# Optimization experiments

Hardware: AMD Instinct MI355X
Metric: run time of the kernel (lower is better)

Reference implementation:

```python
import jax, jax.numpy as jnp
import numpy as np

WINDOW = 1
BETA = 0.01
EPS = 1e-6


def conv3x3(x, W, b):
    y = jax.lax.conv_general_dilated(x, W, (1, 1), 'SAME',
                                     dimension_numbers=('NCHW', 'OIHW', 'NCHW'))
    return y + b[None, :, None, None]


def grid_sample_bilinear(feat, gx, gy):
    # feat [n,C,H,W]; gx,gy [n,h,w] normalized to [-1,1]; align_corners=True, zeros padding
    n, C, H, W = feat.shape
    ix = (gx + 1.0) * 0.5 * (W - 1)
    iy = (gy + 1.0) * 0.5 * (H - 1)
    x0 = jnp.floor(ix)
    y0 = jnp.floor(iy)
    wx = ix - x0
    wy = iy - y0

    def corner(xc, yc, wgt):
        valid = (xc >= 0) & (xc <= W - 1) & (yc >= 0) & (yc <= H - 1)
        xi = jnp.clip(xc, 0, W - 1).astype(jnp.int32)
        yi = jnp.clip(yc, 0, H - 1).astype(jnp.int32)
        g = jax.vmap(lambda f, yy, xx: f[:, yy, xx])(feat, yi, xi)  # [n,C,h,w]
        return g * (wgt * valid)[:, None, :, :]

    return (corner(x0, y0, (1 - wx) * (1 - wy)) +
            corner(x0 + 1, y0, wx * (1 - wy)) +
            corner(x0, y0 + 1, (1 - wx) * wy) +
            corner(x0 + 1, y0 + 1, wx * wy))


def random_pooling(gt, rand, h, w):
    # adaptive_max_pool2d with exact-division output -> uniform block max pool
    n, c, H, W = gt.shape
    kh, kw = H // h, W // w
    rm = rand * (gt > 0.1)
    blocks = rm.reshape(n, c, h, kh, w, kw).transpose(0, 1, 2, 4, 3, 5)
    blocks = blocks.reshape(n, c, h, w, kh * kw)
    loc = jnp.argmax(blocks, axis=-1)
    bi, bj = loc // kw, loc % kw
    row = jnp.arange(h, dtype=jnp.int32)[:, None] * kh + bi
    col = jnp.arange(w, dtype=jnp.int32)[None, :] * kw + bj
    indices = row * W + col  # flat indices into H*W, [n,c,h,w]
    gtf = gt.reshape(n, c, H * W)
    rg = jnp.take_along_axis(gtf, indices.reshape(n, c, h * w), axis=-1)
    rg = rg.reshape(n, c, h, w)
    rg = jnp.where(rg < 0.1, 0.0, rg)
    return rg, indices


def log_grads(rg, window):
    # windowed log-gradients in 4 directions per offset distance
    n, c, h, w = rg.shape
    image = jnp.pad(rg, ((0, 0), (0, 0), (window, window), (window, window)))
    limg = jnp.log(image + EPS)
    mask = image > 0.1
    lc = limg[:, :, window:window + h, window:window + w]
    mc = mask[:, :, window:window + h, window:window + w]
    gs, ms = [], []
    for dd in range(1, window + 1):
        for ox, oy in ((0, dd), (dd, dd), (dd, 0), (dd, -dd)):
            sx, sy = window + ox, window + oy
            gs.append(lc - limg[:, :, sx:sx + h, sy:sy + w])
            ms.append(mc & mask[:, :, sx:sx + h, sy:sy + w])
    return jnp.concatenate(gs, 1), jnp.concatenate(ms, 1)


def single_loss(rand_i, x, d, gts, W_att, b_att, W_post, b_post):
    n, c, h, w = d.shape
    H, W = gts.shape[2], gts.shape[3]
    rg, indices = random_pooling(gts, rand_i, h, w)
    bias = W // w // 2 + (H // h // 2) * W
    indices = indices + bias
    ind_x = 2.0 * ((indices % W).astype(d.dtype) / W - 0.5)
    ind_y = 2.0 * ((indices // W).astype(d.dtype) / H - 0.5)
    feat = grid_sample_bilinear(x, ind_x[:, 0], ind_y[:, 0])
    att = jax.nn.sigmoid(conv3x3(feat, W_att, b_att))
    ds = conv3x3(att * d, W_post, b_post)
    grad_gt, grad_mk = log_grads(rg, WINDOW)
    a = jnp.abs(ds - grad_gt)
    sl1 = jnp.where(a < BETA, 0.5 * a * a / BETA, a - 0.5 * BETA)
    mk = grad_mk.astype(ds.dtype)
    return (sl1 * mk).sum() / mk.sum()


def setup_inputs() -> dict:
    key = jax.random.key(0)
    ks = jax.random.split(key, 8)
    n, H, W = 4, 480, 640
    h, w = 120, 160
    DC, FC, R = 32, 32, 20  # r = 5 * 4 * window
    return {
        'x': jax.random.normal(ks[0], (n, FC, H, W), dtype=jnp.float32),
        'd': jax.random.normal(ks[1], (n, DC, h, w), dtype=jnp.float32),
        'gts': jax.random.uniform(ks[2], (n, 1, H, W), dtype=jnp.float32),
        'rand': jax.random.uniform(ks[3], (R, n, 1, H, W), dtype=jnp.float32),
        'W_att': jax.random.normal(ks[4], (DC, FC, 3, 3), dtype=jnp.float32) * 0.05,
        'b_att': jnp.zeros((DC,), dtype=jnp.float32),
        'W_post': jax.random.normal(ks[5], (4 * WINDOW, DC, 3, 3), dtype=jnp.float32) * 0.05,
        'b_post': jnp.zeros((4 * WINDOW,), dtype=jnp.float32),
    }


def reference(x, d, gts, rand, W_att, b_att, W_post, b_post):
    def step(acc, r_i):
        return acc + single_loss(r_i, x, d, gts, W_att, b_att, W_post, b_post), None
    total, _ = jax.lax.scan(step, jnp.float32(0.0), rand)
    return total / rand.shape[0]
```

## Files before the change

### kernel.cpp

```cpp
#include <hip/hip_runtime.h>
#include <math.h>

#define NN 4
#define FC 32
#define DC 32
#define HH 480
#define WW 640
#define hh 120
#define ww 160
#define RR 20
#define TILE 14
#define ATT 16
#define FT 18
#define BIAS_IDX 1282
#define CP 16
#define PSTR 20
#define ASTR 257
#define LOGEPS -13.815511f
#define MTHR   -8.0f

#define WS_W1T 64
#define WS_W2T 9280
#define WS_WB1 10432
#define WS_WB2 15040
#define WS_RG  20480
#define WS_IDX 1556480
#define WS_XB  3092480
#define XB_COUNT ((size_t)NN * HH * WW * 16)
#define WS_NEED_BYTES (((size_t)WS_XB + XB_COUNT) * 4)

typedef __attribute__((ext_vector_type(8))) short short8;
typedef __attribute__((ext_vector_type(4))) float f32x4;

__device__ __forceinline__ unsigned int bf16pack(float a, float b) {
    unsigned int ua = __float_as_uint(a);
    ua = (ua + 0x7fffu + ((ua >> 16) & 1u)) >> 16;
    unsigned int ub = __float_as_uint(b);
    ub = (ub + 0x7fffu + ((ub >> 16) & 1u)) >> 16;
    return ua | (ub << 16);
}
__device__ __forceinline__ unsigned short bf16r(float f) {
    unsigned int u = __float_as_uint(f);
    u = (u + 0x7fffu + ((u >> 16) & 1u)) >> 16;
    return (unsigned short)u;
}
__device__ __forceinline__ float bf16tof(unsigned short s) {
    return __uint_as_float(((unsigned int)s) << 16);
}

__global__ void prep_kernel(const float* __restrict__ W_att, const float* __restrict__ W_post,
                            float* __restrict__ ws) {
    int tid = threadIdx.x;
    if (tid < 2*RR) ws[tid] = 0.f;
    float* w1t = ws + WS_W1T;
    float* w2t = ws + WS_W2T;
    for (int i = tid; i < 32*32*9; i += blockDim.x) {
        int oc = i / (32*9); int rem = i % (32*9); int c = rem / 9; int tap = rem % 9;
        w1t[(tap*32 + c)*32 + oc] = W_att[i];
    }
    for (int i = tid; i < 4*32*9; i += blockDim.x) {
        int oc = i / (32*9); int rem = i % (32*9); int c = rem / 9; int tap = rem % 9;
        w2t[(tap*32 + c)*4 + oc] = W_post[i];
    }
    unsigned int* wb = (unsigned int*)(ws + WS_WB1);
    for (int i = tid; i < 9*2*64; i += blockDim.x) {
        int lane = i & 63; int th = i >> 6;
        int t = th >> 1, h2 = th & 1;
        int q = lane >> 4, col = lane & 15, oc = h2*16 + col;
        unsigned int vv[4];
        #pragma unroll
        for (int j = 0; j < 4; ++j) {
            int c0 = 8*q + 2*j;
            float f0 = W_att[(oc*32 + c0    )*9 + t];
            float f1 = W_att[(oc*32 + c0 + 1)*9 + t];
            vv[j] = bf16pack(f0, f1);
        }
        uint4 v4; v4.x = vv[0]; v4.y = vv[1]; v4.z = vv[2]; v4.w = vv[3];
        ((uint4*)wb)[i] = v4;
    }
    unsigned int* wb2 = (unsigned int*)(ws + WS_WB2);
    for (int i = tid; i < 9*2*64; i += blockDim.x) {
        int lane = i & 63; int th = i >> 6;
        int t = th >> 1, part = th & 1;
        int q = lane >> 4, oc = lane & 15;
        unsigned int vv[4];
        #pragma unroll
        for (int j = 0; j < 4; ++j) {
            int c0 = 8*q + 2*j;
            float f0 = (oc < 4) ? W_post[(oc*32 + c0    )*9 + t] : 0.f;
            float f1 = (oc < 4) ? W_post[(oc*32 + c0 + 1)*9 + t] : 0.f;
            if (part == 0) {
                vv[j] = ((unsigned int)bf16r(f0)) | (((unsigned int)bf16r(f1)) << 16);
            } else {
                float l0 = f0 - bf16tof(bf16r(f0));
                float l1 = f1 - bf16tof(bf16r(f1));
                vv[j] = ((unsigned int)bf16r(l0)) | (((unsigned int)bf16r(l1)) << 16);
            }
        }
        uint4 v4; v4.x = vv[0]; v4.y = vv[1]; v4.z = vv[2]; v4.w = vv[3];
        ((uint4*)wb2)[i] = v4;
    }
}

__global__ void xpack_kernel(const float* __restrict__ x, unsigned int* __restrict__ xb) {
    const int y = blockIdx.x;
    const int n = blockIdx.y;
    for (int px = threadIdx.x; px < WW; px += 256) {
        unsigned int* o = xb + ((size_t)(n*HH + y)*WW + px) * 16;
        uint4 v[4];
        #pragma unroll
        for (int k = 0; k < 4; ++k) {
            #pragma unroll
            for (int j = 0; j < 4; ++j) {
                int cp = 4*k + j;
                float f0 = x[((size_t)(n*FC + 2*cp    )*HH + y)*WW + px];
                float f1 = x[((size_t)(n*FC + 2*cp + 1)*HH + y)*WW + px];
                ((unsigned int*)&v[k])[j] = bf16pack(f0, f1);
            }
        }
        #pragma unroll
        for (int k = 0; k < 4; ++k) ((uint4*)o)[k] = v[k];
    }
}

__global__ void pool_kernel(const float* __restrict__ gts, const float* __restrict__ rnd,
                            float* __restrict__ ws) {
    const int r = blockIdx.z, n = blockIdx.y;
    const int cell = blockIdx.x * 256 + threadIdx.x;
    const int h = cell / ww, w = cell % ww;
    const float* gt_n = gts + (size_t)n * HH * WW;
    const float* rd_n = rnd + ((size_t)r * NN + n) * (size_t)(HH * WW);
    float best = -1.f, bg = 0.f; int bii = 0, bjj = 0;
    #pragma unroll
    for (int bi = 0; bi < 4; ++bi) {
        const float4 g4 = *(const float4*)(gt_n + (size_t)(h*4 + bi)*WW + w*4);
        const float4 r4 = *(const float4*)(rd_n + (size_t)(h*4 + bi)*WW + w*4);
        const float gv[4] = {g4.x, g4.y, g4.z, g4.w};
        const float rv[4] = {r4.x, r4.y, r4.z, r4.w};
        #pragma unroll
        for (int bj = 0; bj < 4; ++bj) {
            float rm = (gv[bj] > 0.1f) ? rv[bj] : 0.f;
            if (rm > best) { best = rm; bii = bi; bjj = bj; bg = gv[bj]; }
        }
    }
    int idx_b = (h*4 + bii) * WW + (w*4 + bjj) + BIAS_IDX;
    size_t o = ((size_t)(r*NN + n) * (hh*ww)) + cell;
    float g2 = (bg < 0.1f) ? 0.f : bg;
    ((float*)(ws + WS_RG))[o] = logf(g2 + 1e-6f);
    ((unsigned int*)(ws + WS_IDX))[o] = ((unsigned int)(idx_b / WW) << 16) | (unsigned int)(idx_b % WW);
}

__launch_bounds__(256, 5)
__global__ void wvl_main(const unsigned int* __restrict__ xb, const float* __restrict__ d,
                         const float* __restrict__ b_att, const float* __restrict__ b_post,
                         float* __restrict__ ws) {
    __shared__ unsigned int s_feat[FT * FT * PSTR];
    __shared__ float s_plog[FT * FT];
    __shared__ int   s_pidx[FT * FT];
    __shared__ float s_rn[4], s_rd[4];

    const float* lg_all  = (const float*)(ws + WS_RG);
    const unsigned int* pidx_all = (const unsigned int*)(ws + WS_IDX);

    const int tid = threadIdx.x;

    const int f   = blockIdx.x;
    const int xcd = f & 7;
    const int bb  = f >> 3;
    const int gi  = bb / 120;
    const int ii  = bb % 120;
    const int band = gi * 8 + xcd;
    const int n   = band / 18;
    const int rem = band % 18;
    const int ty  = rem >> 1;
    const int tx  = (rem & 1) * 6 + (ii % 6);
    const int r   = ii / 6;

    const int py0 = ty * TILE - 2;
    const int px0 = tx * TILE - 2;

    {
        const size_t base = (size_t)(r*NN + n) * (hh*ww);
        for (int p = tid; p < FT * FT; p += 256) {
            int pi = p / FT, pj = p % FT;
            int gi2 = py0 + pi, gj = px0 + pj;
            float lval = LOGEPS; int pk = -1;
            if (gi2 >= 0 && gi2 < hh && gj >= 0 && gj < ww) {
                size_t o = base + (size_t)gi2 * ww + gj;
                lval = lg_all[o];
                pk = (int)pidx_all[o];
            }
            s_plog[p] = lval;
            s_pidx[p] = pk;
        }
    }
    __syncthreads();

    for (int p = tid; p < FT * FT; p += 256) {
        int pk = s_pidx[p];
        unsigned int* dst = &s_feat[p * PSTR];
        if (pk < 0) {
            uint4 z; z.x = z.y = z.z = z.w = 0u;
            #pragma unroll
            for (int k = 0; k < 4; ++k) ((uint4*)dst)[k] = z;
            continue;
        }
        int rr2 = pk >> 16;
        int cc  = pk & 0xffff;
        float gxf = 2.0f * ((float)cc  / (float)WW - 0.5f);
        float gyf = 2.0f * ((float)rr2 / (float)HH - 0.5f);
        float ix = (gxf + 1.0f) * 0.5f * (float)(WW - 1);
        float iy = (gyf + 1.0f) * 0.5f * (float)(HH - 1);
        float x0f = floorf(ix), y0f = floorf(iy);
        float wx = ix - x0f, wy = iy - y0f;
        int x0 = (int)x0f, y0 = (int)y0f;
        float vx0 = (x0f >= 0.f        && x0f <= (float)(WW-1)) ? 1.f : 0.f;
        float vx1 = (x0f + 1.f >= 0.f  && x0f + 1.f <= (float)(WW-1)) ? 1.f : 0.f;
        float vy0 = (y0f >= 0.f        && y0f <= (float)(HH-1)) ? 1.f : 0.f;
        float vy1 = (y0f + 1.f >= 0.f  && y0f + 1.f <= (float)(HH-1)) ? 1.f : 0.f;
        int xi0 = min(max(x0, 0), WW-1),  xi1 = min(max(x0+1, 0), WW-1);
        int yi0 = min(max(y0, 0), HH-1),  yi1 = min(max(y0+1, 0), HH-1);
        float w00 = (1.f-wx)*(1.f-wy) * (vx0*vy0);
        float w10 = wx*(1.f-wy)       * (vx1*vy0);
        float w01 = (1.f-wx)*wy       * (vx0*vy1);
        float w11 = wx*wy             * (vx1*vy1);
        const uint4* q00 = (const uint4*)(xb + ((size_t)(n*HH + yi0)*WW + xi0) * 16);
        const uint4* q10 = (const uint4*)(xb + ((size_t)(n*HH + yi0)*WW + xi1) * 16);
        const uint4* q01 = (const uint4*)(xb + ((size_t)(n*HH + yi1)*WW + xi0) * 16);
        const uint4* q11 = (const uint4*)(xb + ((size_t)(n*HH + yi1)*WW + xi1) * 16);
        #pragma unroll
        for (int k = 0; k < 4; ++k) {
            uint4 A = q00[k], B = q10[k], C = q01[k], D = q11[k];
            uint4 o;
            #pragma unroll
            for (int j = 0; j < 4; ++j) {
                unsigned int ua = ((const unsigned int*)&A)[j];
                unsigned int ub = ((const unsigned int*)&B)[j];
                unsigned int uc = ((const unsigned int*)&C)[j];
                unsigned int ud = ((const unsigned int*)&D)[j];
                float f0 = w00 * __uint_as_float(ua << 16)
                         + w10 * __uint_as_float(ub << 16)
                         + w01 * __uint_as_float(uc << 16)
                         + w11 * __uint_as_float(ud << 16);
                float f1 = w00 * __uint_as_float(ua & 0xffff0000u)
                         + w10 * __uint_as_float(ub & 0xffff0000u)
                         + w01 * __uint_as_float(uc & 0xffff0000u)
                         + w11 * __uint_as_float(ud & 0xffff0000u);
                ((unsigned int*)&o)[j] = bf16pack(f0, f1);
            }
            ((uint4*)dst)[k] = o;
        }
    }
    __syncthreads();

    const int lane = tid & 63;
    const int wv   = tid >> 6;
    const int mcol = lane & 15;
    const int q    = lane >> 4;

    f32x4 acc1[4][2];
    {
        float bb0 = b_att[mcol];
        float bb1 = b_att[mcol + 16];
        #pragma unroll
        for (int rr = 0; rr < 4; ++rr) {
            acc1[rr][0] = (f32x4){bb0, bb0, bb0, bb0};
            acc1[rr][1] = (f32x4){bb1, bb1, bb1, bb1};
        }
    }
    {
        const uint4* wB = (const uint4*)(ws + WS_WB1);
        #pragma unroll
        for (int t = 0; t < 9; ++t) {
            union { uint4 u; short8 s; } b0u, b1u;
            b0u.u = wB[(t*2 + 0)*64 + lane];
            b1u.u = wB[(t*2 + 1)*64 + lane];
            const int dy = t / 3, dx = t % 3;
            #pragma unroll
            for (int rr = 0; rr < 4; ++rr) {
                int ay = wv*4 + rr;
                int pix = (ay + dy) * FT + dx + mcol;
                union { uint4 u; short8 s; } a;
                a.u = *(const uint4*)&s_feat[pix * PSTR + 4*q];
                acc1[rr][0] = __builtin_amdgcn_mfma_f32_16x16x32_bf16(a.s, b0u.s, acc1[rr][0], 0, 0, 0);
                acc1[rr][1] = __builtin_amdgcn_mfma_f32_16x16x32_bf16(a.s, b1u.s, acc1[rr][1], 0, 0, 0);
            }
        }
    }
    __syncthreads();

    {
        unsigned short* attd16 = (unsigned short*)s_feat;
        #pragma unroll
        for (int rr = 0; rr < 4; ++rr) {
            int ay = wv*4 + rr;
            int gy = ty * TILE - 1 + ay;
            bool gyok = (gy >= 0 && gy < hh);
            #pragma unroll
            for (int h2 = 0; h2 < 2; ++h2) {
                int oc = mcol + 16*h2;
                const float* drow = d + ((size_t)(n*DC + oc) * hh + (gyok ? gy : 0)) * ww;
                #pragma unroll
                for (int reg = 0; reg < 4; ++reg) {
                    int ax = 4*q + reg;
                    int gx = tx * TILE - 1 + ax;
                    float av = 1.f / (1.f + __expf(-acc1[rr][h2][reg]));
                    float dv = (gyok && gx >= 0 && gx < ww) ? drow[gx] : 0.f;
                    int pix = ay * ATT + ax;
                    attd16[(pix * PSTR + (oc >> 1)) * 2 + (oc & 1)] = bf16r(av * dv);
                }
            }
        }
    }
    __syncthreads();

    float num_t = 0.f, den_t = 0.f;
    {
        const uint4* wB2 = (const uint4*)(ws + WS_WB2);
        const int qy0 = wv * 4;
        float bias2 = (mcol < 4) ? b_post[mcol] : 0.f;
        f32x4 acc2[4];
        #pragma unroll
        for (int rr = 0; rr < 4; ++rr) acc2[rr] = (f32x4){bias2, bias2, bias2, bias2};
        #pragma unroll
        for (int t = 0; t < 9; ++t) {
            union { uint4 u; short8 s; } bh, bl;
            bh.u = wB2[(t*2 + 0)*64 + lane];
            bl.u = wB2[(t*2 + 1)*64 + lane];
            const int dy = t / 3, dx = t % 3;
            #pragma unroll
            for (int rr = 0; rr < 4; ++rr) {
                if (qy0 + rr >= TILE) break;
                int pix = (qy0 + rr + dy) * ATT + (mcol + dx);
                union { uint4 u; short8 s; } a;
                a.u = *(const uint4*)&s_feat[pix * PSTR + 4*q];
                acc2[rr] = __builtin_amdgcn_mfma_f32_16x16x32_bf16(a.s, bh.s, acc2[rr], 0, 0, 0);
                acc2[rr] = __builtin_amdgcn_mfma_f32_16x16x32_bf16(a.s, bl.s, acc2[rr], 0, 0, 0);
            }
        }
        const int o3 = mcol & 3;
        const int oy = (o3 == 0) ? 0 : 1;
        const int ox = (o3 == 3) ? -1 : ((o3 == 2) ? 0 : 1);
        #pragma unroll
        for (int rr = 0; rr < 4; ++rr) {
            if (qy0 + rr >= TILE) break;
            int qy = qy0 + rr;
            int gy2 = ty * TILE + qy;
            bool rowok = (gy2 < hh);
            #pragma unroll
            for (int reg = 0; reg < 4; ++reg) {
                int qx = 4*q + reg;
                int gx2 = tx * TILE + qx;
                float lc = s_plog[(qy + 2) * FT + (qx + 2)];
                float ln = s_plog[(qy + 2 + oy) * FT + (qx + 2 + ox)];
                bool m = rowok && (qx < TILE) && (gx2 < ww) && (mcol < 4)
                       && (lc > MTHR) && (ln > MTHR);
                float a2 = fabsf(acc2[rr][reg] - (lc - ln));
                float sl1 = (a2 < 0.01f) ? (50.f * a2 * a2) : (a2 - 0.005f);
                if (m) { num_t += sl1; den_t += 1.f; }
            }
        }
    }

    for (int off = 32; off > 0; off >>= 1) {
        num_t += __shfl_down(num_t, off);
        den_t += __shfl_down(den_t, off);
    }
    if (lane == 0) { s_rn[wv] = num_t; s_rd[wv] = den_t; }
    __syncthreads();
    if (tid == 0) {
        atomicAdd(&ws[r],      s_rn[0] + s_rn[1] + s_rn[2] + s_rn[3]);
        atomicAdd(&ws[RR + r], s_rd[0] + s_rd[1] + s_rd[2] + s_rd[3]);
    }
}

__launch_bounds__(256, 6)
__global__ void wvl_fallback(const float* __restrict__ x, const float* __restrict__ d,
                             const float* __restrict__ gts, const float* __restrict__ rnd,
                             const float* __restrict__ b_att, const float* __restrict__ b_post,
                             float* __restrict__ ws) {
    __shared__ unsigned int s_buf[CP * FT * FT];
    __shared__ float s_pgt[FT * FT];
    __shared__ int   s_pidx[FT * FT];
    __shared__ float s_rn[4], s_rd[4];

    const float* w1t = ws + WS_W1T;
    const float* w2t = ws + WS_W2T;

    const int tid = threadIdx.x;
    const int tilesx = (ww + TILE - 1) / TILE;
    const int tx = blockIdx.x % tilesx;
    const int ty = blockIdx.x / tilesx;
    const int n  = blockIdx.y;
    const int r  = blockIdx.z;
    const int py0 = ty * TILE - 2;
    const int px0 = tx * TILE - 2;

    const float* gt_n = gts + (size_t)n * HH * WW;
    const float* rd_n = rnd + ((size_t)r * NN + n) * (size_t)(HH * WW);
    for (int p = tid; p < FT * FT; p += 256) {
        int pi = p / FT, pj = p % FT;
        int gi = py0 + pi, gj = px0 + pj;
        float gval = 0.f; int idx = -1;
        if (gi >= 0 && gi < hh && gj >= 0 && gj < ww) {
            float best = -1.f; int bii = 0, bjj = 0; float bg = 0.f;
            #pragma unroll
            for (int bi = 0; bi < 4; ++bi) {
                const float* gr = gt_n + (size_t)(gi*4 + bi) * WW + gj*4;
                const float* rp = rd_n + (size_t)(gi*4 + bi) * WW + gj*4;
                #pragma unroll
                for (int bj = 0; bj < 4; ++bj) {
                    float g  = gr[bj];
                    float rv = rp[bj];
                    float rm = (g > 0.1f) ? rv : 0.f;
                    if (rm > best) { best = rm; bii = bi; bjj = bj; bg = g; }
                }
            }
            gval = bg;
            idx = (gi*4 + bii) * WW + (gj*4 + bjj) + BIAS_IDX;
        }
        s_pgt[p]  = gval;
        s_pidx[p] = idx;
    }
    __syncthreads();

    const float* x_n = x + (size_t)n * FC * HH * WW;
    for (int p = tid; p < FT * FT; p += 256) {
        int idx = s_pidx[p];
        if (idx < 0) {
            #pragma unroll
            for (int cp = 0; cp < CP; ++cp) s_buf[cp * (FT*FT) + p] = 0u;
            continue;
        }
        int cc = idx % WW;
        int rr2 = idx / WW;
        float gxf = 2.0f * ((float)cc  / (float)WW - 0.5f);
        float gyf = 2.0f * ((float)rr2 / (float)HH - 0.5f);
        float ix = (gxf + 1.0f) * 0.5f * (float)(WW - 1);
        float iy = (gyf + 1.0f) * 0.5f * (float)(HH - 1);
        float x0f = floorf(ix), y0f = floorf(iy);
        float wx = ix - x0f, wy = iy - y0f;
        int x0 = (int)x0f, y0 = (int)y0f;
        float vx0 = (x0f >= 0.f        && x0f <= (float)(WW-1)) ? 1.f : 0.f;
        float vx1 = (x0f + 1.f >= 0.f  && x0f + 1.f <= (float)(WW-1)) ? 1.f : 0.f;
        float vy0 = (y0f >= 0.f        && y0f <= (float)(HH-1)) ? 1.f : 0.f;
        float vy1 = (y0f + 1.f >= 0.f  && y0f + 1.f <= (float)(HH-1)) ? 1.f : 0.f;
        int xi0 = min(max(x0, 0), WW-1),  xi1 = min(max(x0+1, 0), WW-1);
        int yi0 = min(max(y0, 0), HH-1),  yi1 = min(max(y0+1, 0), HH-1);
        float w00 = (1.f-wx)*(1.f-wy) * (vx0*vy0);
        float w10 = wx*(1.f-wy)       * (vx1*vy0);
        float w01 = (1.f-wx)*wy       * (vx0*vy1);
        float w11 = wx*wy             * (vx1*vy1);
        const float* p00 = x_n + (size_t)yi0 * WW + xi0;
        const float* p10 = x_n + (size_t)yi0 * WW + xi1;
        const float* p01 = x_n + (size_t)yi1 * WW + xi0;
        const float* p11 = x_n + (size_t)yi1 * WW + xi1;
        #pragma unroll 4
        for (int cp = 0; cp < CP; ++cp) {
            int o0 = (2*cp)     * (HH * WW);
            int o1 = (2*cp + 1) * (HH * WW);
            float f0 = w00 * p00[o0] + w10 * p10[o0] + w01 * p01[o0] + w11 * p11[o0];
            float f1 = w00 * p00[o1] + w10 * p10[o1] + w01 * p01[o1] + w11 * p11[o1];
            s_buf[cp * (FT*FT) + p] = bf16pack(f0, f1);
        }
    }
    __syncthreads();

    const int ay = tid >> 4, ax = tid & 15;
    float acc[32];
    #pragma unroll
    for (int oc = 0; oc < 32; ++oc) acc[oc] = b_att[oc];
    for (int dy = 0; dy < 3; ++dy) {
        for (int dx = 0; dx < 3; ++dx) {
            const float* wt = w1t + (dy*3 + dx) * 1024;
            int base = (ay + dy) * FT + (ax + dx);
            for (int cp = 0; cp < CP; ++cp) {
                unsigned int u = s_buf[cp * (FT*FT) + base];
                float f0 = __uint_as_float(u << 16);
                float f1 = __uint_as_float(u & 0xffff0000u);
                const float* wp0 = wt + (2*cp) * 32;
                const float* wp1 = wp0 + 32;
                #pragma unroll
                for (int oc = 0; oc < 32; ++oc) acc[oc] = fmaf(f0, wp0[oc], acc[oc]);
                #pragma unroll
                for (int oc = 0; oc < 32; ++oc) acc[oc] = fmaf(f1, wp1[oc], acc[oc]);
            }
        }
    }
    __syncthreads();
    {
        int gy = ty * TILE - 1 + ay;
        int gx = tx * TILE - 1 + ax;
        bool inb = (gy >= 0 && gy < hh && gx >= 0 && gx < ww);
        const float* d_n = d + (size_t)n * DC * hh * ww;
        #pragma unroll
        for (int cp = 0; cp < CP; ++cp) {
            float a0 = 1.f / (1.f + __expf(-acc[2*cp]));
            float a1 = 1.f / (1.f + __expf(-acc[2*cp+1]));
            float v0 = 0.f, v1 = 0.f;
            if (inb) {
                v0 = a0 * d_n[(size_t)((2*cp)   * hh + gy) * ww + gx];
                v1 = a1 * d_n[(size_t)((2*cp+1) * hh + gy) * ww + gx];
            }
            s_buf[cp * (ATT*ATT) + tid] = bf16pack(v0, v1);
        }
    }
    __syncthreads();

    float num_t = 0.f, den_t = 0.f;
    if (tid < TILE * TILE) {
        int qy = tid / TILE, qx = tid % TILE;
        int gy2 = ty * TILE + qy, gx2 = tx * TILE + qx;
        if (gy2 < hh && gx2 < ww) {
            float acc2[4];
            #pragma unroll
            for (int k = 0; k < 4; ++k) acc2[k] = b_post[k];
            for (int dy = 0; dy < 3; ++dy) {
                for (int dx = 0; dx < 3; ++dx) {
                    const float* wt = w2t + (dy*3 + dx) * 128;
                    int base = (qy + dy) * ATT + (qx + dx);
                    for (int cp = 0; cp < CP; ++cp) {
                        unsigned int u = s_buf[cp * (ATT*ATT) + base];
                        float f0 = __uint_as_float(u << 16);
                        float f1 = __uint_as_float(u & 0xffff0000u);
                        const float* wp0 = wt + (2*cp) * 4;
                        const float* wp1 = wp0 + 4;
                        #pragma unroll
                        for (int k2 = 0; k2 < 4; ++k2) acc2[k2] = fmaf(f0, wp0[k2], acc2[k2]);
                        #pragma unroll
                        for (int k2 = 0; k2 < 4; ++k2) acc2[k2] = fmaf(f1, wp1[k2], acc2[k2]);
                    }
                }
            }
            int pc = (qy + 2) * FT + (qx + 2);
            float rgc = s_pgt[pc]; rgc = (rgc < 0.1f) ? 0.f : rgc;
            float lc = logf(rgc + 1e-6f);
            bool  mc = rgc > 0.1f;
            const int oys[4] = {0, 1, 1, 1};
            const int oxs[4] = {1, 1, 0, -1};
            #pragma unroll
            for (int k = 0; k < 4; ++k) {
                int pnb = (qy + 2 + oys[k]) * FT + (qx + 2 + oxs[k]);
                float rgn = s_pgt[pnb]; rgn = (rgn < 0.1f) ? 0.f : rgn;
                float ln = logf(rgn + 1e-6f);
                bool m = mc && (rgn > 0.1f);
                float gg = lc - ln;
                float a2 = fabsf(acc2[k] - gg);
                float sl1 = (a2 < 0.01f) ? (0.5f * a2 * a2 / 0.01f) : (a2 - 0.005f);
                if (m) { num_t += sl1; den_t += 1.f; }
            }
        }
    }
    for (int off = 32; off > 0; off >>= 1) {
        num_t += __shfl_down(num_t, off);
        den_t += __shfl_down(den_t, off);
    }
    int wid = tid >> 6, lane = tid & 63;
    if (lane == 0) { s_rn[wid] = num_t; s_rd[wid] = den_t; }
    __syncthreads();
    if (tid == 0) {
        atomicAdd(&ws[r],      s_rn[0] + s_rn[1] + s_rn[2] + s_rn[3]);
        atomicAdd(&ws[RR + r], s_rd[0] + s_rd[1] + s_rd[2] + s_rd[3]);
    }
}

__global__ void finish_kernel(const float* __restrict__ ws, float* __restrict__ out) {
    if (threadIdx.x == 0 && blockIdx.x == 0) {
        float s = 0.f;
        for (int r = 0; r < RR; ++r) s += ws[r] / ws[RR + r];
        out[0] = s / (float)RR;
    }
}

extern "C" void kernel_launch(void* const* d_in, const int* in_sizes, int n_in,
                              void* d_out, int out_size, void* d_ws, size_t ws_size,
                              hipStream_t stream) {
    const float* x      = (const float*)d_in[0];
    const float* d      = (const float*)d_in[1];
    const float* gts    = (const float*)d_in[2];
    const float* rnd    = (const float*)d_in[3];
    const float* W_att  = (const float*)d_in[4];
    const float* b_att  = (const float*)d_in[5];
    const float* W_post = (const float*)d_in[6];
    const float* b_post = (const float*)d_in[7];
    float* out = (float*)d_out;
    float* ws  = (float*)d_ws;

    hipLaunchKernelGGL(prep_kernel, dim3(1), dim3(1024), 0, stream, W_att, W_post, ws);

    const int tilesx = (ww + TILE - 1) / TILE;
    const int tilesy = (hh + TILE - 1) / TILE;

    if (ws_size >= WS_NEED_BYTES) {
        unsigned int* xb = (unsigned int*)(ws + WS_XB);
        hipLaunchKernelGGL(xpack_kernel, dim3(HH, NN), dim3(256), 0, stream, x, xb);
        hipLaunchKernelGGL(pool_kernel, dim3(hh*ww/256, NN, RR), dim3(256), 0, stream, gts, rnd, ws);
        hipLaunchKernelGGL(wvl_main, dim3(tilesx * tilesy * NN * RR), dim3(256), 0, stream,
                           xb, d, b_att, b_post, ws);
    } else {
        dim3 grid(tilesx, tilesy * NN * RR);
        dim3 grid2(tilesx * tilesy, NN, RR);
        hipLaunchKernelGGL(wvl_fallback, grid2, dim3(256), 0, stream,
                           x, d, gts, rnd, b_att, b_post, ws);
    }

    hipLaunchKernelGGL(finish_kernel, dim3(1), dim3(64), 0, stream, ws, out);
}
```

Before: 601.8 us.

## Swizzle shared feature tile to shrink LDS and raise occupancy

Replaces the padded shared-memory feature layout (stride 20) with a dense stride-16 layout that uses an XOR swizzle on 16-byte chunks to avoid bank conflicts. It also drops the s_pidx staging array and its barrier by reading pooled indices directly from global memory, and raises the launch-bounds occupancy target from 5 to 7 blocks. Smaller changes vectorize the bilinear blend with float2 math and use a hardware reciprocal in the sigmoid. The higher occupancy target may force register spills, and the swizzle must match across every read and write path.

```diff
diff --git a/kernel.cpp b/kernel.cpp
--- a/kernel.cpp
+++ b/kernel.cpp
@@ -14,7 +14,6 @@
 #define FT 18
 #define BIAS_IDX 1282
 #define CP 16
-#define PSTR 20
 #define ASTR 257
 #define LOGEPS -13.815511f
 #define MTHR   -8.0f
@@ -31,6 +30,7 @@
 
 typedef __attribute__((ext_vector_type(8))) short short8;
 typedef __attribute__((ext_vector_type(4))) float f32x4;
+typedef __attribute__((ext_vector_type(2))) float f32x2;
 
 __device__ __forceinline__ unsigned int bf16pack(float a, float b) {
     unsigned int ua = __float_as_uint(a);
@@ -150,13 +150,12 @@
     ((unsigned int*)(ws + WS_IDX))[o] = ((unsigned int)(idx_b / WW) << 16) | (unsigned int)(idx_b % WW);
 }
 
-__launch_bounds__(256, 5)
+__launch_bounds__(256, 7)
 __global__ void wvl_main(const unsigned int* __restrict__ xb, const float* __restrict__ d,
                          const float* __restrict__ b_att, const float* __restrict__ b_post,
                          float* __restrict__ ws) {
-    __shared__ unsigned int s_feat[FT * FT * PSTR];
+    __shared__ unsigned int s_feat[FT * FT * 16];
     __shared__ float s_plog[FT * FT];
-    __shared__ int   s_pidx[FT * FT];
     __shared__ float s_rn[4], s_rd[4];
 
     const float* lg_all  = (const float*)(ws + WS_RG);
@@ -179,34 +178,31 @@
     const int py0 = ty * TILE - 2;
     const int px0 = tx * TILE - 2;
 
-    {
-        const size_t base = (size_t)(r*NN + n) * (hh*ww);
-        for (int p = tid; p < FT * FT; p += 256) {
-            int pi = p / FT, pj = p % FT;
-            int gi2 = py0 + pi, gj = px0 + pj;
-            float lval = LOGEPS; int pk = -1;
-            if (gi2 >= 0 && gi2 < hh && gj >= 0 && gj < ww) {
-                size_t o = base + (size_t)gi2 * ww + gj;
-                lval = lg_all[o];
-                pk = (int)pidx_all[o];
-            }
-            s_plog[p] = lval;
-            s_pidx[p] = pk;
-        }
-    }
-    __syncthreads();
+    const size_t pbase = (size_t)(r*NN + n) * (hh*ww);
 
     for (int p = tid; p < FT * FT; p += 256) {
-        int pk = s_pidx[p];
-        unsigned int* dst = &s_feat[p * PSTR];
-        if (pk < 0) {
+        int pi = p / FT, pj = p % FT;
+        int gi2 = py0 + pi, gj = px0 + pj;
+        float lval = LOGEPS;
+        if (gi2 >= 0 && gi2 < hh && gj >= 0 && gj < ww)
+            lval = lg_all[pbase + (size_t)gi2 * ww + gj];
+        s_plog[p] = lval;
+    }
+
+    for (int p = tid; p < FT * FT; p += 256) {
+        int pi = p / FT, pj = p % FT;
+        int gi2 = py0 + pi, gj = px0 + pj;
+        unsigned int* dst = &s_feat[p * 16];
+        const int sw = (p >> 1) & 3;
+        if (gi2 < 0 || gi2 >= hh || gj < 0 || gj >= ww) {
             uint4 z; z.x = z.y = z.z = z.w = 0u;
             #pragma unroll
             for (int k = 0; k < 4; ++k) ((uint4*)dst)[k] = z;
             continue;
         }
-        int rr2 = pk >> 16;
-        int cc  = pk & 0xffff;
+        unsigned int pk = pidx_all[pbase + (size_t)gi2 * ww + gj];
+        int rr2 = (int)(pk >> 16);
+        int cc  = (int)(pk & 0xffff);
         float gxf = 2.0f * ((float)cc  / (float)WW - 0.5f);
         float gyf = 2.0f * ((float)rr2 / (float)HH - 0.5f);
         float ix = (gxf + 1.0f) * 0.5f * (float)(WW - 1);
@@ -224,6 +220,7 @@
         float w10 = wx*(1.f-wy)       * (vx1*vy0);
         float w01 = (1.f-wx)*wy       * (vx0*vy1);
         float w11 = wx*wy             * (vx1*vy1);
+        const f32x2 vw00 = {w00, w00}, vw10 = {w10, w10}, vw01 = {w01, w01}, vw11 = {w11, w11};
         const uint4* q00 = (const uint4*)(xb + ((size_t)(n*HH + yi0)*WW + xi0) * 16);
         const uint4* q10 = (const uint4*)(xb + ((size_t)(n*HH + yi0)*WW + xi1) * 16);
         const uint4* q01 = (const uint4*)(xb + ((size_t)(n*HH + yi1)*WW + xi0) * 16);
@@ -238,17 +235,17 @@
                 unsigned int ub = ((const unsigned int*)&B)[j];
                 unsigned int uc = ((const unsigned int*)&C)[j];
                 unsigned int ud = ((const unsigned int*)&D)[j];
-                float f0 = w00 * __uint_as_float(ua << 16)
-                         + w10 * __uint_as_float(ub << 16)
-                         + w01 * __uint_as_float(uc << 16)
-                         + w11 * __uint_as_float(ud << 16);
-                float f1 = w00 * __uint_as_float(ua & 0xffff0000u)
-                         + w10 * __uint_as_float(ub & 0xffff0000u)
-                         + w01 * __uint_as_float(uc & 0xffff0000u)
-                         + w11 * __uint_as_float(ud & 0xffff0000u);
-                ((unsigned int*)&o)[j] = bf16pack(f0, f1);
-            }
-            ((uint4*)dst)[k] = o;
+                f32x2 va = {__uint_as_float(ua << 16), __uint_as_float(ua & 0xffff0000u)};
+                f32x2 vb = {__uint_as_float(ub << 16), __uint_as_float(ub & 0xffff0000u)};
+                f32x2 vc = {__uint_as_float(uc << 16), __uint_as_float(uc & 0xffff0000u)};
+                f32x2 vd = {__uint_as_float(ud << 16), __uint_as_float(ud & 0xffff0000u)};
+                f32x2 acc = vw00 * va;
+                acc += vw10 * vb;
+                acc += vw01 * vc;
+                acc += vw11 * vd;
+                ((unsigned int*)&o)[j] = bf16pack(acc.x, acc.y);
+            }
+            ((uint4*)dst)[k ^ sw] = o;
         }
     }
     __syncthreads();
@@ -281,7 +278,7 @@
                 int ay = wv*4 + rr;
                 int pix = (ay + dy) * FT + dx + mcol;
                 union { uint4 u; short8 s; } a;
-                a.u = *(const uint4*)&s_feat[pix * PSTR + 4*q];
+                a.u = *(const uint4*)&s_feat[pix * 16 + (q ^ ((pix >> 1) & 3)) * 4];
                 acc1[rr][0] = __builtin_amdgcn_mfma_f32_16x16x32_bf16(a.s, b0u.s, acc1[rr][0], 0, 0, 0);
                 acc1[rr][1] = __builtin_amdgcn_mfma_f32_16x16x32_bf16(a.s, b1u.s, acc1[rr][1], 0, 0, 0);
             }
@@ -304,10 +301,11 @@
                 for (int reg = 0; reg < 4; ++reg) {
                     int ax = 4*q + reg;
                     int gx = tx * TILE - 1 + ax;
-                    float av = 1.f / (1.f + __expf(-acc1[rr][h2][reg]));
+                    float av = __builtin_amdgcn_rcpf(1.f + __expf(-acc1[rr][h2][reg]));
                     float dv = (gyok && gx >= 0 && gx < ww) ? drow[gx] : 0.f;
                     int pix = ay * ATT + ax;
-                    attd16[(pix * PSTR + (oc >> 1)) * 2 + (oc & 1)] = bf16r(av * dv);
+                    int dwi = pix * 16 + ((oc >> 3) ^ ((pix >> 1) & 3)) * 4 + ((oc >> 1) & 3);
+                    attd16[dwi * 2 + (oc & 1)] = bf16r(av * dv);
                 }
             }
         }
@@ -333,7 +331,7 @@
                 if (qy0 + rr >= TILE) break;
                 int pix = (qy0 + rr + dy) * ATT + (mcol + dx);
                 union { uint4 u; short8 s; } a;
-                a.u = *(const uint4*)&s_feat[pix * PSTR + 4*q];
+                a.u = *(const uint4*)&s_feat[pix * 16 + (q ^ ((pix >> 1) & 3)) * 4];
                 acc2[rr] = __builtin_amdgcn_mfma_f32_16x16x32_bf16(a.s, bh.s, acc2[rr], 0, 0, 0);
                 acc2[rr] = __builtin_amdgcn_mfma_f32_16x16x32_bf16(a.s, bl.s, acc2[rr], 0, 0, 0);
             }
@@ -598,7 +596,6 @@
         hipLaunchKernelGGL(wvl_main, dim3(tilesx * tilesy * NN * RR), dim3(256), 0, stream,
                            xb, d, b_att, b_post, ws);
     } else {
-        dim3 grid(tilesx, tilesy * NN * RR);
         dim3 grid2(tilesx * tilesy, NN, RR);
         hipLaunchKernelGGL(wvl_fallback, grid2, dim3(256), 0, stream,
                            x, d, gts, rnd, b_att, b_post, ws);
```

Result: slower. 858.0 us (+42.6%).
